# Kernel optimization log

Measured on AMD Instinct MI355X. Metric: run time of the kernel, lower is better.

## Reference

```python
import jax, jax.numpy as jnp
import numpy as np

N, E, IN_C, EDGE_D = 100000, 1600000, 16, 4
H1, C1 = 4, 16   # conv1: heads, out channels -> 64
H2, C2 = 4, 16   # conv2: heads, out channels -> 64
G = 64           # num graphs
NUM_MIX, ACTION_DIM, GMM_HID = 3, 10, 64
NEG_SLOPE = 0.2  # PyG GATv2Conv default LeakyReLU slope


def gatv2_layer(x, src, dst, edge_attr, Wl, Wr, We, att, bias, n_nodes, heads, ch):
    # x: [N, Fin] -> out: [N, heads*ch]. Message = alpha * (Wl x)[src];
    # attention logits = att . LeakyReLU((Wl x)[src] + (Wr x)[dst] + We e).
    xl = (x @ Wl).reshape(n_nodes, heads, ch)
    xr = (x @ Wr).reshape(n_nodes, heads, ch)
    ef = (edge_attr @ We).reshape(-1, heads, ch)
    s = jax.nn.leaky_relu(xl[src] + xr[dst] + ef, NEG_SLOPE)      # [E,H,C]
    logits = jnp.einsum('ehc,hc->eh', s, att)                      # [E,H]
    m = jax.ops.segment_max(logits, dst, num_segments=n_nodes)     # [N,H]
    ex = jnp.exp(logits - m[dst])
    denom = jax.ops.segment_sum(ex, dst, num_segments=n_nodes)     # [N,H]
    alpha = ex / denom[dst]                                        # segment softmax over in-edges
    msg = alpha[..., None] * xl[src]                               # [E,H,C]
    out = jax.ops.segment_sum(msg, dst, num_segments=n_nodes)      # [N,H,C]
    return out.reshape(n_nodes, heads * ch) + bias


def global_mean_pool(x, batch, num_graphs):
    s = jax.ops.segment_sum(x, batch, num_segments=num_graphs)
    cnt = jax.ops.segment_sum(jnp.ones((x.shape[0],), x.dtype), batch, num_segments=num_graphs)
    return s / jnp.maximum(cnt, 1.0)[:, None]


def setup_inputs() -> dict:
    key = jax.random.key(0)
    ks = jax.random.split(key, 24)
    sc = 0.1
    x = jax.random.normal(ks[0], (N, IN_C), jnp.float32)
    edge_index = jax.random.randint(ks[1], (2, E), 0, N, jnp.int64)
    edge_attr = jax.random.normal(ks[2], (E, EDGE_D), jnp.float32)
    batch = jnp.sort(jax.random.randint(ks[3], (N,), 0, G, jnp.int64))
    p = {}
    p['Wl1'] = jax.random.normal(ks[4], (IN_C, H1 * C1), jnp.float32) * sc
    p['Wr1'] = jax.random.normal(ks[5], (IN_C, H1 * C1), jnp.float32) * sc
    p['We1'] = jax.random.normal(ks[6], (EDGE_D, H1 * C1), jnp.float32) * sc
    p['att1'] = jax.random.normal(ks[7], (H1, C1), jnp.float32) * sc
    p['b1'] = jnp.zeros((H1 * C1,), jnp.float32)
    p['Wl2'] = jax.random.normal(ks[8], (H1 * C1, H2 * C2), jnp.float32) * sc
    p['Wr2'] = jax.random.normal(ks[9], (H1 * C1, H2 * C2), jnp.float32) * sc
    p['We2'] = jax.random.normal(ks[10], (EDGE_D, H2 * C2), jnp.float32) * sc
    p['att2'] = jax.random.normal(ks[11], (H2, C2), jnp.float32) * sc
    p['b2'] = jnp.zeros((H2 * C2,), jnp.float32)
    p['Wg1'] = jax.random.normal(ks[12], (H2 * C2, GMM_HID), jnp.float32) * sc
    p['bg1'] = jnp.zeros((GMM_HID,), jnp.float32)
    p['Wg2'] = jax.random.normal(ks[13], (GMM_HID, NUM_MIX * 5), jnp.float32) * sc
    p['bg2'] = jnp.zeros((NUM_MIX * 5,), jnp.float32)
    p['Wp'] = jax.random.normal(ks[14], (H2 * C2, ACTION_DIM), jnp.float32) * sc
    p['bp'] = jnp.zeros((ACTION_DIM,), jnp.float32)
    p['Wc1'] = jax.random.normal(ks[15], (H2 * C2, 64), jnp.float32) * sc
    p['bc1'] = jnp.zeros((64,), jnp.float32)
    p['Wc2'] = jax.random.normal(ks[16], (64, 1), jnp.float32) * sc
    p['bc2'] = jnp.zeros((1,), jnp.float32)
    return dict(x=x, edge_index=edge_index, edge_attr=edge_attr, batch=batch, **p)


def reference(x, edge_index, edge_attr, batch,
              Wl1, Wr1, We1, att1, b1,
              Wl2, Wr2, We2, att2, b2,
              Wg1, bg1, Wg2, bg2, Wp, bp, Wc1, bc1, Wc2, bc2):
    src, dst = edge_index[0], edge_index[1]
    y = gatv2_layer(x, src, dst, edge_attr, Wl1, Wr1, We1, att1, b1, N, H1, C1)
    y = jax.nn.elu(y)
    # dropout is identity in eval mode
    y = gatv2_layer(y, src, dst, edge_attr, Wl2, Wr2, We2, att2, b2, N, H2, C2)
    g = global_mean_pool(y, batch, G)                      # [G, H2*C2]
    gmm_params = jax.nn.relu(g @ Wg1 + bg1) @ Wg2 + bg2    # [G, 15]
    num_proposals_logits = g @ Wp + bp                     # [G, 10]
    values = (jax.nn.relu(g @ Wc1 + bc1) @ Wc2 + bc2)[:, 0]  # [G]
    return gmm_params, num_proposals_logits, values
```

## Files before the change

### kernel.cpp

```cpp
#include <hip/hip_runtime.h>

#define DEVINL __device__ __forceinline__

#if __has_builtin(__builtin_amdgcn_exp2f)
DEVINL float fexp2(float x) { return __builtin_amdgcn_exp2f(x); }
#else
DEVINL float fexp2(float x) { return exp2f(x); }
#endif

DEVINL float red4(float pv) {
    pv += __int_as_float(__builtin_amdgcn_ds_swizzle(__float_as_int(pv), 0x041F));
    pv += __int_as_float(__builtin_amdgcn_ds_swizzle(__float_as_int(pv), 0x081F));
    return pv;
}

template <int K>
__global__ void k_lin_tiled(const float* __restrict__ x,
                            const float* __restrict__ Wa,
                            const float* __restrict__ Wb,
                            float* __restrict__ oa, float* __restrict__ ob,
                            int N) {
    __shared__ float sx[64 * K];
    __shared__ float sw[K * 128];
    int t = threadIdx.x;
    int base = blockIdx.x * 64;

    const int WTOT = K * 64 / 4;
    for (int i = t; i < WTOT; i += 256) {
        float4 wa = ((const float4*)Wa)[i];
        float4 wb = ((const float4*)Wb)[i];
        int k = (i * 4) >> 6, f = (i * 4) & 63;
        *(float4*)&sw[k * 128 + f] = wa;
        *(float4*)&sw[k * 128 + 64 + f] = wb;
    }
    const int XTOT = 64 * K / 4;
    for (int i = t; i < XTOT; i += 256) {
        int n = (i * 4) / K, kk = (i * 4) % K;
        float4 v = make_float4(0.f, 0.f, 0.f, 0.f);
        if (base + n < N) v = *(const float4*)&x[(size_t)(base + n) * K + kk];
        *(float4*)&sx[n * K + kk] = v;
    }
    __syncthreads();

    int fq = t & 31;
    int nq = t >> 5;
    float acc[8][4];
#pragma unroll
    for (int i = 0; i < 8; ++i)
#pragma unroll
        for (int c = 0; c < 4; ++c) acc[i][c] = 0.f;

    for (int k0 = 0; k0 < K; k0 += 4) {
        float4 xv[8];
#pragma unroll
        for (int i = 0; i < 8; ++i)
            xv[i] = *(const float4*)&sx[(nq * 8 + i) * K + k0];
#pragma unroll
        for (int kk = 0; kk < 4; ++kk) {
            float4 w = *(const float4*)&sw[(k0 + kk) * 128 + fq * 4];
#pragma unroll
            for (int i = 0; i < 8; ++i) {
                float xs = (kk == 0) ? xv[i].x : (kk == 1) ? xv[i].y
                         : (kk == 2) ? xv[i].z : xv[i].w;
                acc[i][0] = fmaf(xs, w.x, acc[i][0]);
                acc[i][1] = fmaf(xs, w.y, acc[i][1]);
                acc[i][2] = fmaf(xs, w.z, acc[i][2]);
                acc[i][3] = fmaf(xs, w.w, acc[i][3]);
            }
        }
    }

    int col = fq * 4;
    float* o = (col < 64) ? oa : ob;
    int c = col & 63;
#pragma unroll
    for (int i = 0; i < 8; ++i) {
        int n = base + nq * 8 + i;
        if (n < N)
            *(float4*)&o[(size_t)n * 64 + c] =
                make_float4(acc[i][0], acc[i][1], acc[i][2], acc[i][3]);
    }
}

__global__ void k_deg(const int* __restrict__ dst, int* __restrict__ deg, int E) {
    int e = blockIdx.x * blockDim.x + threadIdx.x;
    if (e < E) atomicAdd(&deg[dst[e]], 1);
}

__global__ void k_scan1(const int* __restrict__ deg, int* __restrict__ spart,
                        int* __restrict__ bsum, int N) {
    __shared__ int sh[256];
    int base = blockIdx.x * 1024;
    int t = threadIdx.x;
    int v[4]; int sum = 0;
#pragma unroll
    for (int i = 0; i < 4; ++i) {
        int idx = base + t * 4 + i;
        v[i] = (idx < N) ? deg[idx] : 0;
        sum += v[i];
    }
    sh[t] = sum;
    __syncthreads();
    for (int off = 1; off < 256; off <<= 1) {
        int x = (t >= off) ? sh[t - off] : 0;
        __syncthreads();
        sh[t] += x;
        __syncthreads();
    }
    int run = (t > 0) ? sh[t - 1] : 0;
#pragma unroll
    for (int i = 0; i < 4; ++i) {
        run += v[i];
        int idx = base + t * 4 + i;
        if (idx < N) spart[idx] = run;
    }
    if (t == 255) bsum[blockIdx.x] = sh[255];
}

__global__ void k_scan2(int* __restrict__ bsum, int nb) {
    __shared__ int sh[128];
    int t = threadIdx.x;
    sh[t] = (t < nb) ? bsum[t] : 0;
    __syncthreads();
    for (int off = 1; off < 128; off <<= 1) {
        int x = (t >= off) ? sh[t - off] : 0;
        __syncthreads();
        sh[t] += x;
        __syncthreads();
    }
    if (t < nb) bsum[t] = (t > 0) ? sh[t - 1] : 0;
}

__global__ void k_scan3(const int* __restrict__ spart, const int* __restrict__ bsum,
                        int* __restrict__ rowptr, int N) {
    int i = blockIdx.x * blockDim.x + threadIdx.x;
    if (i < N) rowptr[i + 1] = spart[i] + bsum[i >> 10];
    if (i == 0) rowptr[0] = 0;
}

template <bool PACKED>
__global__ void k_scatter(const int* __restrict__ src, const int* __restrict__ dst,
                          const float4* __restrict__ ea,
                          const int* __restrict__ rowptr, int* __restrict__ fill,
                          float4* __restrict__ rec, int* __restrict__ csr_src, int E) {
    int e = blockIdx.x * blockDim.x + threadIdx.x;
    if (e >= E) return;
    int d = dst[e];
    float4 a = ea[e];
    int s = src[e];
    int pos = rowptr[d] + atomicAdd(&fill[d], 1);
    if (PACKED) {
        rec[(size_t)pos * 2] = a;
        *(int*)(rec + (size_t)pos * 2 + 1) = s;
    } else {
        rec[pos] = a;
        csr_src[pos] = s;
    }
}

template <bool PACKED>
__global__ void k_gat_agg(const int* __restrict__ rowptr,
                          const float4* __restrict__ rec,
                          const int* __restrict__ csr_src,
                          const float* __restrict__ xl,
                          const float* __restrict__ xr,
                          const float* __restrict__ We,
                          const float* __restrict__ att,
                          const float* __restrict__ bias,
                          float* __restrict__ out,
                          int N, int elu) {
    int l = threadIdx.x & 63;
    int n = blockIdx.x * 4 + (threadIdx.x >> 6);
    if (n >= N) return;
    int q = l & 15;
    int g = l >> 4;
    int f4 = q * 4;
    const float LOG2E = 1.44269504088896f;

    float4 w0 = *(const float4*)&We[f4];
    float4 w1 = *(const float4*)&We[64 + f4];
    float4 w2 = *(const float4*)&We[128 + f4];
    float4 w3 = *(const float4*)&We[192 + f4];
    float4 at = *(const float4*)&att[f4];
    at.x *= LOG2E; at.y *= LOG2E; at.z *= LOG2E; at.w *= LOG2E;
    float4 xr4 = *(const float4*)&xr[(size_t)n * 64 + f4];

    int beg = rowptr[n], end = rowptr[n + 1];
    const float4* xl4 = (const float4*)xl;

    float m = -1e30f, den = 0.f;
    float4 acc = make_float4(0.f, 0.f, 0.f, 0.f);

    for (int jb = beg; jb < end; jb += 4) {
        int j = jb + g;
        bool valid = (j < end);
        int jj = valid ? j : end - 1;
        float4 a; int s;
        if (PACKED) {
            a = rec[(size_t)jj * 2];
            s = *(const int*)(rec + (size_t)jj * 2 + 1);
        } else {
            a = rec[jj];
            s = csr_src[jj];
        }
        float4 xv = xl4[(unsigned)s * 16u + (unsigned)q];
        float vx = fmaf(a.x, w0.x, fmaf(a.y, w1.x, fmaf(a.z, w2.x, fmaf(a.w, w3.x, xr4.x)))) + xv.x;
        float vy = fmaf(a.x, w0.y, fmaf(a.y, w1.y, fmaf(a.z, w2.y, fmaf(a.w, w3.y, xr4.y)))) + xv.y;
        float vz = fmaf(a.x, w0.z, fmaf(a.y, w1.z, fmaf(a.z, w2.z, fmaf(a.w, w3.z, xr4.z)))) + xv.z;
        float vw = fmaf(a.x, w0.w, fmaf(a.y, w1.w, fmaf(a.z, w2.w, fmaf(a.w, w3.w, xr4.w)))) + xv.w;
        vx = fmaxf(vx, 0.2f * vx);
        vy = fmaxf(vy, 0.2f * vy);
        vz = fmaxf(vz, 0.2f * vz);
        vw = fmaxf(vw, 0.2f * vw);
        float pv = fmaf(vx, at.x, fmaf(vy, at.y, fmaf(vz, at.z, vw * at.w)));
        pv = red4(pv);
        pv = valid ? pv : -3.0e38f;
        float mn = fmaxf(m, pv);
        float sc = fexp2(m - mn);
        float e  = fexp2(pv - mn);
        den = fmaf(den, sc, e);
        acc.x = fmaf(e, xv.x, acc.x * sc);
        acc.y = fmaf(e, xv.y, acc.y * sc);
        acc.z = fmaf(e, xv.z, acc.z * sc);
        acc.w = fmaf(e, xv.w, acc.w * sc);
        m = mn;
    }

#pragma unroll
    for (int mask = 16; mask <= 32; mask <<= 1) {
        float m2 = __shfl_xor(m, mask);
        float d2 = __shfl_xor(den, mask);
        float ax = __shfl_xor(acc.x, mask);
        float ay = __shfl_xor(acc.y, mask);
        float az = __shfl_xor(acc.z, mask);
        float aw = __shfl_xor(acc.w, mask);
        float mn = fmaxf(m, m2);
        float s1 = fexp2(m - mn);
        float s2 = fexp2(m2 - mn);
        den = den * s1 + d2 * s2;
        acc.x = acc.x * s1 + ax * s2;
        acc.y = acc.y * s1 + ay * s2;
        acc.z = acc.z * s1 + az * s2;
        acc.w = acc.w * s1 + aw * s2;
        m = mn;
    }

    float inv = (den > 0.f) ? 1.f / den : 0.f;
    float4 b4 = *(const float4*)&bias[f4];
    float4 val;
    val.x = fmaf(acc.x, inv, b4.x);
    val.y = fmaf(acc.y, inv, b4.y);
    val.z = fmaf(acc.z, inv, b4.z);
    val.w = fmaf(acc.w, inv, b4.w);
    if (elu) {
        val.x = (val.x > 0.f) ? val.x : expm1f(val.x);
        val.y = (val.y > 0.f) ? val.y : expm1f(val.y);
        val.z = (val.z > 0.f) ? val.z : expm1f(val.z);
        val.w = (val.w > 0.f) ? val.w : expm1f(val.w);
    }
    if (l < 16) ((float4*)out)[(size_t)n * 16 + q] = val;
}

__global__ void k_pool(const float* __restrict__ y2,
                       const int* __restrict__ batch,
                       float* __restrict__ pool, float* __restrict__ cnt, int N) {
    const int CH = 256;
    int f = threadIdx.x & 63;
    int lane = threadIdx.x >> 6;
    int base = blockIdx.x * CH;
    int curg = -1;
    float acc = 0.f;
    float c = 0.f;
    for (int n = base + lane; n < base + CH && n < N; n += 4) {
        int g = batch[n];
        if (g != curg) {
            if (curg >= 0) {
                atomicAdd(pool + (size_t)curg * 64 + f, acc);
                if (f == 0) atomicAdd(cnt + curg, c);
            }
            curg = g; acc = 0.f; c = 0.f;
        }
        acc += y2[(size_t)n * 64 + f];
        c += 1.f;
    }
    if (curg >= 0) {
        atomicAdd(pool + (size_t)curg * 64 + f, acc);
        if (f == 0) atomicAdd(cnt + curg, c);
    }
}

__global__ void k_head(const float* __restrict__ pool, const float* __restrict__ cnt,
                       const float* __restrict__ Wg1, const float* __restrict__ bg1,
                       const float* __restrict__ Wg2, const float* __restrict__ bg2,
                       const float* __restrict__ Wp, const float* __restrict__ bp,
                       const float* __restrict__ Wc1, const float* __restrict__ bc1,
                       const float* __restrict__ Wc2, const float* __restrict__ bc2,
                       float* __restrict__ out) {
    int g = blockIdx.x, f = threadIdx.x;
    __shared__ float sg[64];
    __shared__ float sh[64];
    float inv = 1.f / fmaxf(cnt[g], 1.f);
    sg[f] = pool[(size_t)g * 64 + f] * inv;
    __syncthreads();
    float acc = bg1[f];
    for (int k = 0; k < 64; ++k) acc += sg[k] * Wg1[k * 64 + f];
    sh[f] = fmaxf(acc, 0.f);
    __syncthreads();
    if (f < 15) {
        float o = bg2[f];
        for (int k = 0; k < 64; ++k) o += sh[k] * Wg2[k * 15 + f];
        out[(size_t)g * 15 + f] = o;
    }
    if (f < 10) {
        float o = bp[f];
        for (int k = 0; k < 64; ++k) o += sg[k] * Wp[k * 10 + f];
        out[960 + (size_t)g * 10 + f] = o;
    }
    __syncthreads();
    float acc2 = bc1[f];
    for (int k = 0; k < 64; ++k) acc2 += sg[k] * Wc1[k * 64 + f];
    sh[f] = fmaxf(acc2, 0.f);
    __syncthreads();
    if (f == 0) {
        float v = bc2[0];
        for (int k = 0; k < 64; ++k) v += sh[k] * Wc2[k];
        out[1600 + g] = v;
    }
}

extern "C" void kernel_launch(void* const* d_in, const int* in_sizes, int n_in,
                              void* d_out, int out_size, void* d_ws, size_t ws_size,
                              hipStream_t stream) {
    const float* x     = (const float*)d_in[0];
    const int*   ei    = (const int*)d_in[1];
    const float* ea    = (const float*)d_in[2];
    const int*   batch = (const int*)d_in[3];
    const float* Wl1 = (const float*)d_in[4];
    const float* Wr1 = (const float*)d_in[5];
    const float* We1 = (const float*)d_in[6];
    const float* att1 = (const float*)d_in[7];
    const float* b1  = (const float*)d_in[8];
    const float* Wl2 = (const float*)d_in[9];
    const float* Wr2 = (const float*)d_in[10];
    const float* We2 = (const float*)d_in[11];
    const float* att2 = (const float*)d_in[12];
    const float* b2  = (const float*)d_in[13];
    const float* Wg1 = (const float*)d_in[14];
    const float* bg1 = (const float*)d_in[15];
    const float* Wg2 = (const float*)d_in[16];
    const float* bg2 = (const float*)d_in[17];
    const float* Wp  = (const float*)d_in[18];
    const float* bp  = (const float*)d_in[19];
    const float* Wc1 = (const float*)d_in[20];
    const float* bc1 = (const float*)d_in[21];
    const float* Wc2 = (const float*)d_in[22];
    const float* bc2 = (const float*)d_in[23];

    const int N = in_sizes[0] / 16;
    const int E = in_sizes[2] / 4;
    const int* src = ei;
    const int* dst = ei + E;

    size_t NF = (size_t)N * 64;
    size_t tail = ((size_t)(N + 1) + N + N + 128 + 4096 + 64) * 4;
    size_t need_packed = 3 * NF * 4 + (size_t)E * 32 + tail;
    bool packed = (ws_size >= need_packed);

    char* w = (char*)d_ws;
    float* A = (float*)w; w += NF * 4;
    float* B = (float*)w; w += NF * 4;
    float* C = (float*)w; w += NF * 4;
    float4* rec; int* csr_src;
    if (packed) {
        rec = (float4*)w; w += (size_t)E * 32; csr_src = nullptr;
    } else {
        rec = (float4*)w; w += (size_t)E * 16;
        csr_src = (int*)w; w += (size_t)E * 4;
    }
    int* rowptr = (int*)w; w += (size_t)(N + 1) * 4;
    int* deg    = (int*)w; w += (size_t)N * 4;
    int* spart  = (int*)w; w += (size_t)N * 4;
    int* bsum   = (int*)w; w += 128 * 4;
    float* PL   = (float*)w; w += 4096 * 4;
    float* CT   = (float*)w;

    dim3 blk(256);
    int gE  = (E + 255) / 256;
    int gN  = (N + 255) / 256;
    int nb1 = (N + 1023) / 1024;
    int gAgg = (N + 3) / 4;
    int gLin = (N + 63) / 64;

    hipMemsetAsync(deg, 0, (size_t)N * sizeof(int), stream);
    k_deg<<<gE, blk, 0, stream>>>(dst, deg, E);
    k_scan1<<<nb1, blk, 0, stream>>>(deg, spart, bsum, N);
    k_scan2<<<1, 128, 0, stream>>>(bsum, nb1);
    k_scan3<<<gN, blk, 0, stream>>>(spart, bsum, rowptr, N);
    hipMemsetAsync(deg, 0, (size_t)N * sizeof(int), stream);
    if (packed)
        k_scatter<true><<<gE, blk, 0, stream>>>(src, dst, (const float4*)ea,
                                                rowptr, deg, rec, csr_src, E);
    else
        k_scatter<false><<<gE, blk, 0, stream>>>(src, dst, (const float4*)ea,
                                                 rowptr, deg, rec, csr_src, E);

    k_lin_tiled<16><<<gLin, blk, 0, stream>>>(x, Wl1, Wr1, A, B, N);
    if (packed)
        k_gat_agg<true><<<gAgg, blk, 0, stream>>>(rowptr, rec, csr_src, A, B,
                                                  We1, att1, b1, C, N, 1);
    else
        k_gat_agg<false><<<gAgg, blk, 0, stream>>>(rowptr, rec, csr_src, A, B,
                                                   We1, att1, b1, C, N, 1);

    k_lin_tiled<64><<<gLin, blk, 0, stream>>>(C, Wl2, Wr2, B, A, N);
    if (packed)
        k_gat_agg<true><<<gAgg, blk, 0, stream>>>(rowptr, rec, csr_src, B, A,
                                                  We2, att2, b2, C, N, 0);
    else
        k_gat_agg<false><<<gAgg, blk, 0, stream>>>(rowptr, rec, csr_src, B, A,
                                                   We2, att2, b2, C, N, 0);

    hipMemsetAsync(PL, 0, (4096 + 64) * sizeof(float), stream);
    k_pool<<<(N + 255) / 256, blk, 0, stream>>>(C, batch, PL, CT, N);
    k_head<<<64, 64, 0, stream>>>(PL, CT, Wg1, bg1, Wg2, bg2, Wp, bp,
                                  Wc1, bc1, Wc2, bc2, (float*)d_out);
}
```

Before: 462.0 us.

## Two-pass radix partition of edges by destination bucket before CSR scatter

Replaces the single random-scatter CSR build with a two-pass scheme. The first pass partitions edges into about 512 coarse destination buckets, using per-block shared-memory histograms and a staging buffer that reuses the node feature buffers. The second pass scatters each bucket into its final CSR slot, so writes and atomics stay within a small address range. This targets the poor locality of scattering 1.6M 32-byte records across the whole array, at the cost of an extra read/write pass over the edge data and several more launches. It also drops the unpacked fallback, so the workspace must always hold packed records.

```diff
diff --git a/kernel.cpp b/kernel.cpp
--- a/kernel.cpp
+++ b/kernel.cpp
@@ -138,30 +138,80 @@
     if (i == 0) rowptr[0] = 0;
 }
 
-template <bool PACKED>
+__global__ void k_binit(const int* __restrict__ rowptr, int* __restrict__ bfill,
+                        int shift, int B, int N) {
+    int b = blockIdx.x * blockDim.x + threadIdx.x;
+    if (b < B) {
+        long long node = (long long)b << shift;
+        if (node > N) node = N;
+        bfill[b] = rowptr[node];
+    }
+}
+
+__global__ void k_part(const int* __restrict__ src, const int* __restrict__ dst,
+                       const float4* __restrict__ ea,
+                       int* __restrict__ bfill, float4* __restrict__ stg,
+                       int shift, int E, int chunk) {
+    __shared__ int hist[512];
+    __shared__ int base[512];
+    int t = threadIdx.x;
+    int e0 = blockIdx.x * chunk;
+    int e1 = e0 + chunk; if (e1 > E) e1 = E;
+    for (int i = t; i < 512; i += 256) hist[i] = 0;
+    __syncthreads();
+    for (int e = e0 + t; e < e1; e += 256)
+        atomicAdd(&hist[(unsigned)dst[e] >> shift], 1);
+    __syncthreads();
+    for (int i = t; i < 512; i += 256) {
+        int h = hist[i];
+        base[i] = h ? atomicAdd(&bfill[i], h) : 0;
+    }
+    __syncthreads();
+    for (int i = t; i < 512; i += 256) hist[i] = 0;
+    __syncthreads();
+    for (int e = e0 + t; e < e1; e += 256) {
+        int d = dst[e];
+        int b = (unsigned)d >> shift;
+        int off = atomicAdd(&hist[b], 1);
+        size_t pos = (size_t)(base[b] + off);
+        stg[pos * 2] = ea[e];
+        stg[pos * 2 + 1] = make_float4(__int_as_float(src[e]), __int_as_float(d), 0.f, 0.f);
+    }
+}
+
+__global__ void k_scat2(const float4* __restrict__ stg,
+                        const int* __restrict__ rowptr, int* __restrict__ fill,
+                        float4* __restrict__ rec, int shift, int N, int E) {
+    int b = blockIdx.x;
+    long long n0 = (long long)b << shift; if (n0 > N) n0 = N;
+    long long n1 = (long long)(b + 1) << shift; if (n1 > N) n1 = N;
+    int s0 = rowptr[n0], s1 = rowptr[n1];
+    for (int i = s0 + (int)threadIdx.x; i < s1; i += 256) {
+        float4 a = stg[(size_t)i * 2];
+        float4 meta = stg[(size_t)i * 2 + 1];
+        int d = __float_as_int(meta.y);
+        int pos = rowptr[d] + atomicAdd(&fill[d], 1);
+        rec[(size_t)pos * 2] = a;
+        rec[(size_t)pos * 2 + 1] = make_float4(meta.x, 0.f, 0.f, 0.f);
+    }
+}
+
 __global__ void k_scatter(const int* __restrict__ src, const int* __restrict__ dst,
                           const float4* __restrict__ ea,
                           const int* __restrict__ rowptr, int* __restrict__ fill,
-                          float4* __restrict__ rec, int* __restrict__ csr_src, int E) {
+                          float4* __restrict__ rec, int E) {
     int e = blockIdx.x * blockDim.x + threadIdx.x;
     if (e >= E) return;
     int d = dst[e];
     float4 a = ea[e];
     int s = src[e];
     int pos = rowptr[d] + atomicAdd(&fill[d], 1);
-    if (PACKED) {
-        rec[(size_t)pos * 2] = a;
-        *(int*)(rec + (size_t)pos * 2 + 1) = s;
-    } else {
-        rec[pos] = a;
-        csr_src[pos] = s;
-    }
-}
-
-template <bool PACKED>
+    rec[(size_t)pos * 2] = a;
+    rec[(size_t)pos * 2 + 1] = make_float4(__int_as_float(s), 0.f, 0.f, 0.f);
+}
+
 __global__ void k_gat_agg(const int* __restrict__ rowptr,
                           const float4* __restrict__ rec,
-                          const int* __restrict__ csr_src,
                           const float* __restrict__ xl,
                           const float* __restrict__ xr,
                           const float* __restrict__ We,
@@ -195,14 +245,8 @@
         int j = jb + g;
         bool valid = (j < end);
         int jj = valid ? j : end - 1;
-        float4 a; int s;
-        if (PACKED) {
-            a = rec[(size_t)jj * 2];
-            s = *(const int*)(rec + (size_t)jj * 2 + 1);
-        } else {
-            a = rec[jj];
-            s = csr_src[jj];
-        }
+        float4 a = rec[(size_t)jj * 2];
+        int s = *(const int*)(rec + (size_t)jj * 2 + 1);
         float4 xv = xl4[(unsigned)s * 16u + (unsigned)q];
         float vx = fmaf(a.x, w0.x, fmaf(a.y, w1.x, fmaf(a.z, w2.x, fmaf(a.w, w3.x, xr4.x)))) + xv.x;
         float vy = fmaf(a.x, w0.y, fmaf(a.y, w1.y, fmaf(a.z, w2.y, fmaf(a.w, w3.y, xr4.y)))) + xv.y;
@@ -361,28 +405,28 @@
     const int* src = ei;
     const int* dst = ei + E;
 
+    int shift = 8;
+    while (((N + (1 << shift) - 1) >> shift) > 512) ++shift;
+    int B = (N + (1 << shift) - 1) >> shift;
+
     size_t NF = (size_t)N * 64;
-    size_t tail = ((size_t)(N + 1) + N + N + 128 + 4096 + 64) * 4;
-    size_t need_packed = 3 * NF * 4 + (size_t)E * 32 + tail;
-    bool packed = (ws_size >= need_packed);
+    size_t tail = ((size_t)(N + 1) + N + N + 128 + 513 + 4096 + 64) * 4;
+    size_t need = 3 * NF * 4 + (size_t)E * 32 + tail;
+    bool radix = (ws_size >= need) && (2 * NF * 4 >= (size_t)E * 32);
 
     char* w = (char*)d_ws;
     float* A = (float*)w; w += NF * 4;
-    float* B = (float*)w; w += NF * 4;
+    float* B_ = (float*)w; w += NF * 4;
     float* C = (float*)w; w += NF * 4;
-    float4* rec; int* csr_src;
-    if (packed) {
-        rec = (float4*)w; w += (size_t)E * 32; csr_src = nullptr;
-    } else {
-        rec = (float4*)w; w += (size_t)E * 16;
-        csr_src = (int*)w; w += (size_t)E * 4;
-    }
+    float4* rec = (float4*)w; w += (size_t)E * 32;
     int* rowptr = (int*)w; w += (size_t)(N + 1) * 4;
     int* deg    = (int*)w; w += (size_t)N * 4;
     int* spart  = (int*)w; w += (size_t)N * 4;
     int* bsum   = (int*)w; w += 128 * 4;
+    int* bfill  = (int*)w; w += 513 * 4;
     float* PL   = (float*)w; w += 4096 * 4;
     float* CT   = (float*)w;
+    float4* stg = (float4*)A;
 
     dim3 blk(256);
     int gE  = (E + 255) / 256;
@@ -397,28 +441,23 @@
     k_scan2<<<1, 128, 0, stream>>>(bsum, nb1);
     k_scan3<<<gN, blk, 0, stream>>>(spart, bsum, rowptr, N);
     hipMemsetAsync(deg, 0, (size_t)N * sizeof(int), stream);
-    if (packed)
-        k_scatter<true><<<gE, blk, 0, stream>>>(src, dst, (const float4*)ea,
-                                                rowptr, deg, rec, csr_src, E);
-    else
-        k_scatter<false><<<gE, blk, 0, stream>>>(src, dst, (const float4*)ea,
-                                                 rowptr, deg, rec, csr_src, E);
-
-    k_lin_tiled<16><<<gLin, blk, 0, stream>>>(x, Wl1, Wr1, A, B, N);
-    if (packed)
-        k_gat_agg<true><<<gAgg, blk, 0, stream>>>(rowptr, rec, csr_src, A, B,
-                                                  We1, att1, b1, C, N, 1);
-    else
-        k_gat_agg<false><<<gAgg, blk, 0, stream>>>(rowptr, rec, csr_src, A, B,
-                                                   We1, att1, b1, C, N, 1);
-
-    k_lin_tiled<64><<<gLin, blk, 0, stream>>>(C, Wl2, Wr2, B, A, N);
-    if (packed)
-        k_gat_agg<true><<<gAgg, blk, 0, stream>>>(rowptr, rec, csr_src, B, A,
-                                                  We2, att2, b2, C, N, 0);
-    else
-        k_gat_agg<false><<<gAgg, blk, 0, stream>>>(rowptr, rec, csr_src, B, A,
-                                                   We2, att2, b2, C, N, 0);
+    if (radix) {
+        k_binit<<<(B + 255) / 256, blk, 0, stream>>>(rowptr, bfill, shift, B, N);
+        int gridA = 512;
+        int chunk = (E + gridA - 1) / gridA;
+        k_part<<<gridA, blk, 0, stream>>>(src, dst, (const float4*)ea, bfill,
+                                          stg, shift, E, chunk);
+        k_scat2<<<B, blk, 0, stream>>>(stg, rowptr, deg, rec, shift, N, E);
+    } else {
+        k_scatter<<<gE, blk, 0, stream>>>(src, dst, (const float4*)ea,
+                                          rowptr, deg, rec, E);
+    }
+
+    k_lin_tiled<16><<<gLin, blk, 0, stream>>>(x, Wl1, Wr1, A, B_, N);
+    k_gat_agg<<<gAgg, blk, 0, stream>>>(rowptr, rec, A, B_, We1, att1, b1, C, N, 1);
+
+    k_lin_tiled<64><<<gLin, blk, 0, stream>>>(C, Wl2, Wr2, B_, A, N);
+    k_gat_agg<<<gAgg, blk, 0, stream>>>(rowptr, rec, B_, A, We2, att2, b2, C, N, 0);
 
     hipMemsetAsync(PL, 0, (4096 + 64) * sizeof(float), stream);
     k_pool<<<(N + 255) / 256, blk, 0, stream>>>(C, batch, PL, CT, N);
```

New measurement: 485.3 us. 1.05x slower.
